# Kernel optimization log

Hardware: AMD Instinct MI355X
Metric: run time of the kernel (lower is better)

The kernel has to match this reference:

```python
import jax, jax.numpy as jnp
import numpy as np

H_DIM = 256
N_HEADS = 8
HEAD_DIM = H_DIM // N_HEADS
B, N = 2, 2048
LN_EPS = 1e-5


def setup_inputs() -> dict:
    key = jax.random.key(0)
    ks = jax.random.split(key, 20)
    s = 1.0 / np.sqrt(H_DIM)
    inp = {
        'hidden': jax.random.normal(ks[0], (B, N, H_DIM), jnp.float32),
        'adjacency': jax.random.uniform(ks[1], (B, N, N), jnp.float32),
        'positions': jax.random.uniform(ks[2], (B, N, 2), jnp.float32),
        # linear weights stored as (in, out): y = x @ W + b
        'wq': jax.random.normal(ks[3], (H_DIM, H_DIM), jnp.float32) * s,
        'bq': jnp.zeros((H_DIM,), jnp.float32),
        'wk': jax.random.normal(ks[4], (H_DIM, H_DIM), jnp.float32) * s,
        'bk': jnp.zeros((H_DIM,), jnp.float32),
        'wv': jax.random.normal(ks[5], (H_DIM, H_DIM), jnp.float32) * s,
        'bv': jnp.zeros((H_DIM,), jnp.float32),
        'wo': jax.random.normal(ks[6], (H_DIM, H_DIM), jnp.float32) * s,
        'bo': jnp.zeros((H_DIM,), jnp.float32),
        'g1': jnp.ones((H_DIM,), jnp.float32),
        'b1': jnp.zeros((H_DIM,), jnp.float32),
        'g2': jnp.ones((H_DIM,), jnp.float32),
        'b2': jnp.zeros((H_DIM,), jnp.float32),
        'w_ff1': jax.random.normal(ks[7], (H_DIM, 4 * H_DIM), jnp.float32) * s,
        'b_ff1': jnp.zeros((4 * H_DIM,), jnp.float32),
        'w_ff2': jax.random.normal(ks[8], (4 * H_DIM, H_DIM), jnp.float32) * (1.0 / np.sqrt(4 * H_DIM)),
        'b_ff2': jnp.zeros((H_DIM,), jnp.float32),
    }
    return inp


def _layernorm(x, g, b):
    mu = jnp.mean(x, axis=-1, keepdims=True)
    var = jnp.var(x, axis=-1, keepdims=True)
    return (x - mu) * jax.lax.rsqrt(var + LN_EPS) * g + b


def reference(hidden, adjacency, positions, wq, bq, wk, bk, wv, bv, wo, bo,
              g1, b1, g2, b2, w_ff1, b_ff1, w_ff2, b_ff2):
    b_, n_, _ = hidden.shape
    normalized = _layernorm(hidden, g1, b1)
    # project and split heads: [B, H, N, Dh]
    def heads(x):
        return x.reshape(b_, n_, N_HEADS, HEAD_DIM).transpose(0, 2, 1, 3)
    q = heads(normalized @ wq + bq)
    k = heads(normalized @ wk + bk)
    v = heads(normalized @ wv + bv)
    logits = jnp.einsum('bhnd,bhmd->bhnm', q, k) / np.sqrt(HEAD_DIM)
    cond = adjacency[:, None, :, :]  # mode == 'connectivity'
    logits = logits + (2.0 * cond - 1.0)
    weights = jax.nn.softmax(logits, axis=-1)
    weights = weights * (0.25 + 0.75 * cond)
    weights = weights / jnp.maximum(weights.sum(axis=-1, keepdims=True), 1e-6)
    attended = jnp.einsum('bhnm,bhmd->bhnd', weights, v)
    attended = attended.transpose(0, 2, 1, 3).reshape(b_, n_, H_DIM)
    hidden = hidden + attended @ wo + bo
    h2 = _layernorm(hidden, g2, b2)
    ff = jax.nn.gelu(h2 @ w_ff1 + b_ff1, approximate=False) @ w_ff2 + b_ff2
    return hidden + ff
```

## Files before the change

### kernel.cpp

```cpp
#include <hip/hip_runtime.h>
#include <math.h>

#define BB 2
#define NN 2048
#define HD 256
#define NH 8
#define DH 32
#define NTOK (BB*NN)
#define QKVLD 768
#define NSPLIT 2
#define KVPB (NN/NSPLIT)
#define NTILES (KVPB/64)

typedef _Float16 h8 __attribute__((ext_vector_type(8)));
typedef _Float16 h4 __attribute__((ext_vector_type(4)));
typedef float fx4 __attribute__((ext_vector_type(4)));

#define LOG2E 1.4426950408889634f
#define SQ_LOG2 0.25503486f
#define C1A (2.0f * LOG2E)
#define C0A (-(LOG2E + 6.0f))

__device__ __forceinline__ void ln_row(const float* __restrict__ x,
    const float* __restrict__ g, const float* __restrict__ bta,
    _Float16* __restrict__ yh, int row, int lane)
{
  const float* xr = x + (size_t)row * HD + lane * 4;
  float4 v = *(const float4*)xr;
  float s = v.x + v.y + v.z + v.w;
  #pragma unroll
  for (int off = 32; off > 0; off >>= 1) s += __shfl_xor(s, off);
  float mu = s * (1.0f / HD);
  float dx0 = v.x - mu, dx1 = v.y - mu, dx2 = v.z - mu, dx3 = v.w - mu;
  float ss = dx0*dx0 + dx1*dx1 + dx2*dx2 + dx3*dx3;
  #pragma unroll
  for (int off = 32; off > 0; off >>= 1) ss += __shfl_xor(ss, off);
  float rinv = rsqrtf(ss * (1.0f / HD) + 1e-5f);
  float4 gv = *(const float4*)(g   + lane * 4);
  float4 bv = *(const float4*)(bta + lane * 4);
  h4 hh;
  hh[0] = (_Float16)(dx0 * rinv * gv.x + bv.x);
  hh[1] = (_Float16)(dx1 * rinv * gv.y + bv.y);
  hh[2] = (_Float16)(dx2 * rinv * gv.z + bv.z);
  hh[3] = (_Float16)(dx3 * rinv * gv.w + bv.w);
  *(h4*)(yh + (size_t)row * HD + lane * 4) = hh;
}

__global__ __launch_bounds__(256) void ln_kernel(const float* __restrict__ x,
    const float* __restrict__ g, const float* __restrict__ bta,
    _Float16* __restrict__ yh)
{
  ln_row(x, g, bta, yh, blockIdx.x * 4 + (threadIdx.x >> 6), threadIdx.x & 63);
}

__device__ __forceinline__ void do_transpose(const float* __restrict__ W,
    _Float16* __restrict__ Wh, int Nw, int rowoff, int ldout, float scale,
    int bx, int by, float (*tile)[33])
{
  int k0 = by * 32, n0 = bx * 32;
  int c = threadIdx.x & 31, r = threadIdx.x >> 5;
  #pragma unroll
  for (int i = 0; i < 4; i++)
    tile[r + i * 8][c] = W[(size_t)(k0 + r + i * 8) * Nw + n0 + c];
  __syncthreads();
  #pragma unroll
  for (int i = 0; i < 4; i++) {
    int n = r + i * 8;
    Wh[(size_t)(rowoff + n0 + n) * ldout + k0 + c] = (_Float16)(tile[c][n] * scale);
  }
}

__global__ __launch_bounds__(256) void prep_kernel(
    const float* wq, const float* wk, const float* wv, const float* wo,
    const float* wf1, const float* wf2,
    const float* bq, const float* bk, const float* bv,
    const float* hidden, const float* g1, const float* b1,
    _Float16* WtQKVh, _Float16* WtOh, _Float16* WtF1h, _Float16* WtF2h,
    float* biasqkv, _Float16* norm1h)
{
  __shared__ float tile[32][33];
  int bid = blockIdx.x;
  if (bid < 64)        do_transpose(wq,  WtQKVh,  256,   0,  256, SQ_LOG2, bid & 7, bid >> 3, tile);
  else if (bid < 128)  do_transpose(wk,  WtQKVh,  256, 256,  256, 1.0f, (bid-64) & 7, (bid-64) >> 3, tile);
  else if (bid < 192)  do_transpose(wv,  WtQKVh,  256, 512,  256, 1.0f, (bid-128) & 7, (bid-128) >> 3, tile);
  else if (bid < 256)  do_transpose(wo,  WtOh,    256,   0,  256, 1.0f, (bid-192) & 7, (bid-192) >> 3, tile);
  else if (bid < 512)  do_transpose(wf1, WtF1h,  1024,   0,  256, 1.0f, (bid-256) & 31, (bid-256) >> 5, tile);
  else if (bid < 768)  do_transpose(wf2, WtF2h,   256,   0, 1024, 1.0f, (bid-512) & 7, (bid-512) >> 3, tile);
  else if (bid == 768) {
    #pragma unroll
    for (int j = 0; j < 3; j++) {
      int t = j * 256 + threadIdx.x;
      biasqkv[t] = (t < 256) ? bq[t] * SQ_LOG2 : (t < 512) ? bk[t - 256] : bv[t - 512];
    }
  } else {
    ln_row(hidden, g1, b1, norm1h, (bid - 769) * 4 + (threadIdx.x >> 6), threadIdx.x & 63);
  }
}

template<int KK, int NT, int NX, int ACT, int RES, int OM>
__global__ __launch_bounds__(256) void gemm16_kernel(
    const _Float16* __restrict__ Ah, const _Float16* __restrict__ Wh,
    const float* __restrict__ bias, const float* __restrict__ resid,
    float* __restrict__ Cf, _Float16* __restrict__ Ch,
    _Float16* __restrict__ vtb, int N)
{
  const int lin = blockIdx.x;
  const int qch = gridDim.x >> 3;
  const int wg = (lin & 7) * qch + (lin >> 3);
  const int bx = wg % NX, by = wg / NX;
  const int n0 = bx * (NT * 16);
  const int m0 = by * 64;
  const int t = threadIdx.x, w = t >> 6, l = t & 63;
  const int ml = l & 15, g = l >> 4;
  const int mrow = m0 + w * 16 + ml;

  const _Float16* aph = Ah + (size_t)mrow * KK + g * 8;
  const _Float16* whp[NT];
  #pragma unroll
  for (int nt = 0; nt < NT; nt++)
    whp[nt] = Wh + (size_t)(n0 + nt * 16 + ml) * KK + g * 8;

  fx4 acc[NT];
  #pragma unroll
  for (int nt = 0; nt < NT; nt++) acc[nt] = (fx4){0.f, 0.f, 0.f, 0.f};

  h8 ah = *(const h8*)(aph);
  h8 wh[NT];
  #pragma unroll
  for (int nt = 0; nt < NT; nt++) wh[nt] = *(const h8*)(whp[nt]);

  #pragma unroll 2
  for (int k0 = 32; k0 <= KK; k0 += 32) {
    h8 ahn;
    h8 whn[NT];
    if (k0 < KK) {
      ahn = *(const h8*)(aph + k0);
      #pragma unroll
      for (int nt = 0; nt < NT; nt++) whn[nt] = *(const h8*)(whp[nt] + k0);
    }
    #pragma unroll
    for (int nt = 0; nt < NT; nt++)
      acc[nt] = __builtin_amdgcn_mfma_f32_16x16x32_f16(ah, wh[nt], acc[nt], 0, 0, 0);
    ah = ahn;
    #pragma unroll
    for (int nt = 0; nt < NT; nt++) wh[nt] = whn[nt];
  }

  #pragma unroll
  for (int nt = 0; nt < NT; nt++) {
    int n = n0 + nt * 16 + ml;
    float bv = bias[n];
    #pragma unroll
    for (int i = 0; i < 4; i++) {
      int m = m0 + w * 16 + 4 * g + i;
      float vv = acc[nt][i] + bv;
      if (ACT == 1) vv = 0.5f * vv * (1.0f + erff(vv * 0.70710678118654752f));
      if (RES)      vv += resid[(size_t)m * N + n];
      if (OM == 0) {
        Cf[(size_t)m * N + n] = vv;
      } else if (OM == 1) {
        Ch[(size_t)m * N + n] = (_Float16)vv;
      } else {
        if (n < 512) Ch[(size_t)m * QKVLD + n] = (_Float16)vv;
        else {
          int dim = n - 512, kv = m & (NN - 1), bb = m >> 11;
          int kvp = (kv & ~31) | ((kv & 15) << 1) | ((kv >> 4) & 1);
          vtb[((size_t)(bb * HD + dim)) * NN + kvp] = (_Float16)vv;
        }
      }
    }
  }
}

__global__ __launch_bounds__(256) void wo_fused_kernel(
    const _Float16* __restrict__ Opart, const float* __restrict__ Spart,
    const _Float16* __restrict__ Wh, const float* __restrict__ bias,
    const float* __restrict__ resid, float* __restrict__ Cf)
{
  const int lin = blockIdx.x;
  const int qch = gridDim.x >> 3;
  const int wg = (lin & 7) * qch + (lin >> 3);
  const int bx = wg & 7, by = wg >> 3;
  const int n0 = bx * 32;
  const int m0 = by * 64;
  const int t = threadIdx.x, w = t >> 6, l = t & 63;
  const int ml = l & 15, g = l >> 4;
  const int mrow = m0 + w * 16 + ml;
  const int bb = mrow >> 11, qrow = mrow & (NN - 1);

  const _Float16* whp0 = Wh + (size_t)(n0 + ml) * HD + g * 8;
  const _Float16* whp1 = Wh + (size_t)(n0 + 16 + ml) * HD + g * 8;

  fx4 acc0 = {0.f, 0.f, 0.f, 0.f};
  fx4 acc1 = {0.f, 0.f, 0.f, 0.f};

  #pragma unroll
  for (int h = 0; h < NH; h++) {
    size_t p0 = ((size_t)((bb * 2 + 0) * NH + h)) * NN + qrow;
    size_t p1 = ((size_t)((bb * 2 + 1) * NH + h)) * NN + qrow;
    float s0 = Spart[p0], s1 = Spart[p1];
    float den = 1.0f / (s0 + s1);
    float w0 = s0 * den, w1 = s1 * den;
    h8 o0 = *(const h8*)(Opart + p0 * 32 + g * 8);
    h8 o1 = *(const h8*)(Opart + p1 * 32 + g * 8);
    h8 ah;
    #pragma unroll
    for (int j = 0; j < 8; j++)
      ah[j] = (_Float16)(w0 * (float)o0[j] + w1 * (float)o1[j]);
    h8 wh0 = *(const h8*)(whp0 + h * 32);
    h8 wh1 = *(const h8*)(whp1 + h * 32);
    acc0 = __builtin_amdgcn_mfma_f32_16x16x32_f16(ah, wh0, acc0, 0, 0, 0);
    acc1 = __builtin_amdgcn_mfma_f32_16x16x32_f16(ah, wh1, acc1, 0, 0, 0);
  }

  #pragma unroll
  for (int i = 0; i < 4; i++) {
    int m = m0 + w * 16 + 4 * g + i;
    int na = n0 + ml, nb = n0 + 16 + ml;
    Cf[(size_t)m * HD + na] = acc0[i] + bias[na] + resid[(size_t)m * HD + na];
    Cf[(size_t)m * HD + nb] = acc1[i] + bias[nb] + resid[(size_t)m * HD + nb];
  }
}

__global__ __launch_bounds__(512) void attn_mfma_kernel(
    const _Float16* __restrict__ qkv16, const _Float16* __restrict__ vtb,
    const float* __restrict__ adj,
    _Float16* __restrict__ Opart, float* __restrict__ Spart)
{
  __shared__ _Float16 Ksh[2][2][64][40];
  __shared__ _Float16 Vp[2][2][32][72];
  __shared__ _Float16 AdjL[2][64][68];

  const int z = blockIdx.z;
  const int b = z >> 1, half = z & 1;
  const int hg = blockIdx.y;
  const int q0 = blockIdx.x * 64;
  const int t = threadIdx.x;
  const int hh_ = t >> 8;
  const int head = hg * 2 + hh_;
  const int tl = t & 255;
  const int w = tl >> 6, l = t & 63;
  const int m = l & 15, g = l >> 4;
  const int kvbase = half * KVPB;

  const int qrow = q0 + w * 16 + m;
  h8 qh = *(const h8*)(qkv16 + ((size_t)(b * NN + qrow)) * QKVLD + head * DH + g * 8);

  fx4 ot0 = {0.f, 0.f, 0.f, 0.f};
  fx4 ot1 = {0.f, 0.f, 0.f, 0.f};
  float S4[4] = {0.f, 0.f, 0.f, 0.f};

  const int arow0 = t >> 4;
  const int acol = (t & 15) * 4;
  const float* adjbase = adj + ((size_t)(b * NN + q0)) * NN + kvbase;

  const int krow = tl >> 2, kd0 = (tl & 3) * 8;
  const int vdim = tl >> 3, vkc = (tl & 7) * 8;
  const _Float16* kbase = qkv16 + ((size_t)(b * NN + kvbase + krow)) * QKVLD + 256 + head * DH + kd0;
  const _Float16* vbase = vtb + ((size_t)(b * HD + head * DH + vdim)) * NN + kvbase + vkc;

  h8 kreg = *(const h8*)kbase;
  h8 vreg = *(const h8*)vbase;

  {
    float4 ar[2];
    #pragma unroll
    for (int j = 0; j < 2; j++)
      ar[j] = *(const float4*)(adjbase + (size_t)(j * 32 + arow0) * NN + acol);
    #pragma unroll
    for (int j = 0; j < 2; j++) {
      h4 hh;
      hh[0] = (_Float16)ar[j].x; hh[1] = (_Float16)ar[j].y;
      hh[2] = (_Float16)ar[j].z; hh[3] = (_Float16)ar[j].w;
      *(h4*)&AdjL[0][j * 32 + arow0][acol] = hh;
    }
  }
  *(h8*)&Ksh[hh_][0][krow][kd0] = kreg;
  *(h8*)&Vp[hh_][0][vdim][vkc]  = vreg;
  kreg = *(const h8*)(kbase + (size_t)64 * QKVLD);
  vreg = *(const h8*)(vbase + 64);
  __syncthreads();

  for (int tt = 0; tt < NTILES; ++tt) {
    const int cur = tt & 1;

    float4 ar[2];
    if (tt + 1 < NTILES) {
      #pragma unroll
      for (int j = 0; j < 2; j++)
        ar[j] = *(const float4*)(adjbase + (size_t)(j * 32 + arow0) * NN
                                 + (tt + 1) * 64 + acol);
    }

    h8 kh0 = *(const h8*)&Ksh[hh_][cur][     m][g * 8];
    h8 kh1 = *(const h8*)&Ksh[hh_][cur][16 + m][g * 8];
    h8 kh2 = *(const h8*)&Ksh[hh_][cur][32 + m][g * 8];
    h8 kh3 = *(const h8*)&Ksh[hh_][cur][48 + m][g * 8];
    fx4 z4 = {0.f, 0.f, 0.f, 0.f};
    fx4 st[4];
    st[0] = __builtin_amdgcn_mfma_f32_16x16x32_f16(kh0, qh, z4, 0, 0, 0);
    st[1] = __builtin_amdgcn_mfma_f32_16x16x32_f16(kh1, qh, z4, 0, 0, 0);
    st[2] = __builtin_amdgcn_mfma_f32_16x16x32_f16(kh2, qh, z4, 0, 0, 0);
    st[3] = __builtin_amdgcn_mfma_f32_16x16x32_f16(kh3, qh, z4, 0, 0, 0);

    float pv[16];
    #pragma unroll
    for (int p = 0; p < 4; p++) {
      h4 ah4 = *(const h4*)&AdjL[cur][w * 16 + m][p * 16 + g * 4];
      float ps = 0.f;
      #pragma unroll
      for (int i = 0; i < 4; i++) {
        float a = (float)ah4[i];
        float e = __builtin_amdgcn_exp2f(st[p][i] + C1A * a + C0A);
        float pp = (0.25f + 0.75f * a) * e;
        pv[p * 4 + i] = pp;
        ps += pp;
      }
      S4[p] += ps;
    }
    h8 ph0, ph1;
    #pragma unroll
    for (int q2 = 0; q2 < 4; q2++) {
      ph0[2*q2]     = (_Float16)pv[q2];
      ph0[2*q2 + 1] = (_Float16)pv[4 + q2];
      ph1[2*q2]     = (_Float16)pv[8 + q2];
      ph1[2*q2 + 1] = (_Float16)pv[12 + q2];
    }

    h8 v00 = *(const h8*)&Vp[hh_][cur][m][g * 8];
    h8 v01 = *(const h8*)&Vp[hh_][cur][m][32 + g * 8];
    h8 v10 = *(const h8*)&Vp[hh_][cur][16 + m][g * 8];
    h8 v11 = *(const h8*)&Vp[hh_][cur][16 + m][32 + g * 8];
    ot0 = __builtin_amdgcn_mfma_f32_16x16x32_f16(v00, ph0, ot0, 0, 0, 0);
    ot0 = __builtin_amdgcn_mfma_f32_16x16x32_f16(v01, ph1, ot0, 0, 0, 0);
    ot1 = __builtin_amdgcn_mfma_f32_16x16x32_f16(v10, ph0, ot1, 0, 0, 0);
    ot1 = __builtin_amdgcn_mfma_f32_16x16x32_f16(v11, ph1, ot1, 0, 0, 0);

    if (tt + 1 < NTILES) {
      #pragma unroll
      for (int j = 0; j < 2; j++) {
        h4 hh;
        hh[0] = (_Float16)ar[j].x; hh[1] = (_Float16)ar[j].y;
        hh[2] = (_Float16)ar[j].z; hh[3] = (_Float16)ar[j].w;
        *(h4*)&AdjL[cur ^ 1][j * 32 + arow0][acol] = hh;
      }
      *(h8*)&Ksh[hh_][cur ^ 1][krow][kd0] = kreg;
      *(h8*)&Vp[hh_][cur ^ 1][vdim][vkc]  = vreg;
      if (tt + 2 < NTILES) {
        kreg = *(const h8*)(kbase + (size_t)((tt + 2) * 64) * QKVLD);
        vreg = *(const h8*)(vbase + (tt + 2) * 64);
      }
    }
    __syncthreads();
  }

  float S = (S4[0] + S4[1]) + (S4[2] + S4[3]);
  S += __shfl_xor(S, 16);
  S += __shfl_xor(S, 32);

  float is = 1.0f / S;
  size_t prow = ((size_t)(z * NH + head)) * NN + qrow;
  _Float16* po = Opart + prow * 32;
  h4 o0h, o1h;
  #pragma unroll
  for (int j = 0; j < 4; j++) {
    o0h[j] = (_Float16)(ot0[j] * is);
    o1h[j] = (_Float16)(ot1[j] * is);
  }
  *(h4*)(po + 4 * g)      = o0h;
  *(h4*)(po + 16 + 4 * g) = o1h;
  if (g == 0) Spart[prow] = S;
}

extern "C" void kernel_launch(void* const* d_in, const int* in_sizes, int n_in,
                              void* d_out, int out_size, void* d_ws, size_t ws_size,
                              hipStream_t stream)
{
  const float* hidden    = (const float*)d_in[0];
  const float* adjacency = (const float*)d_in[1];
  const float* wq  = (const float*)d_in[3];
  const float* bq  = (const float*)d_in[4];
  const float* wk  = (const float*)d_in[5];
  const float* bk  = (const float*)d_in[6];
  const float* wv  = (const float*)d_in[7];
  const float* bv  = (const float*)d_in[8];
  const float* wo  = (const float*)d_in[9];
  const float* bo  = (const float*)d_in[10];
  const float* g1  = (const float*)d_in[11];
  const float* b1  = (const float*)d_in[12];
  const float* g2  = (const float*)d_in[13];
  const float* b2  = (const float*)d_in[14];
  const float* wf1 = (const float*)d_in[15];
  const float* bf1 = (const float*)d_in[16];
  const float* wf2 = (const float*)d_in[17];
  const float* bf2 = (const float*)d_in[18];
  float* out = (float*)d_out;

  char* base = (char*)d_ws;
  const size_t MB = 1024 * 1024;
  _Float16* norm1h = (_Float16*)(base);
  _Float16* qkv16  = (_Float16*)(base + 2*MB);
  _Float16* vtb    = (_Float16*)(base + 8*MB);
  float*    hid2   = (float*)(base + 12*MB);
  _Float16* Opart = (_Float16*)(base + 16*MB);
  _Float16* ffah  = (_Float16*)(base + 16*MB);
  float* Spart = (float*)(base + 25*MB);
  _Float16* wtb = (_Float16*)(base + 26*MB);
  _Float16* WtQKVh = wtb; wtb += 768 * 256;
  _Float16* WtOh   = wtb; wtb += 256 * 256;
  _Float16* WtF1h  = wtb; wtb += 1024 * 256;
  _Float16* WtF2h  = wtb; wtb += 256 * 1024;
  float* biasqkv = (float*)(base + 28*MB);

  prep_kernel<<<1793, 256, 0, stream>>>(wq, wk, wv, wo, wf1, wf2, bq, bk, bv,
      hidden, g1, b1, WtQKVh, WtOh, WtF1h, WtF2h, biasqkv, norm1h);

  gemm16_kernel<256, 4, 12, 0, 0, 2><<<768, 256, 0, stream>>>(
      norm1h, WtQKVh, biasqkv, nullptr, nullptr, qkv16, vtb, QKVLD);

  attn_mfma_kernel<<<dim3(NN / 64, NH / 2, BB * NSPLIT), 512, 0, stream>>>(
      qkv16, vtb, adjacency, Opart, Spart);

  wo_fused_kernel<<<512, 256, 0, stream>>>(
      Opart, Spart, WtOh, bo, hidden, hid2);

  ln_kernel<<<NTOK / 4, 256, 0, stream>>>(hid2, g2, b2, norm1h);

  gemm16_kernel<256, 4, 16, 1, 0, 1><<<1024, 256, 0, stream>>>(
      norm1h, WtF1h, bf1, nullptr, nullptr, ffah, nullptr, 1024);

  gemm16_kernel<1024, 4, 4, 0, 1, 0><<<256, 256, 0, stream>>>(
      ffah, WtF2h, bf2, hid2, out, nullptr, nullptr, 256);
}
```

Measured before the change: 112.7 us.

## Drop KV split in attention and use generic GEMM for output projection

Removes the two-way split of the key/value range in attention, so each block processes the full sequence and writes final normalized head outputs directly into a token-major fp16 buffer. The custom wo_fused kernel that merged partial outputs with their softmax sums is replaced by the generic gemm16 kernel, with bias and residual added. This drops the partial-output writes and reads and the merge arithmetic. In exchange the attention grid is halved to 256 blocks, each with twice the serial KV loop, which may reduce occupancy and latency hiding on a device with many CUs.

```diff
diff --git a/kernel.cpp b/kernel.cpp
--- a/kernel.cpp
+++ b/kernel.cpp
@@ -8,9 +8,7 @@
 #define DH 32
 #define NTOK (BB*NN)
 #define QKVLD 768
-#define NSPLIT 2
-#define KVPB (NN/NSPLIT)
-#define NTILES (KVPB/64)
+#define NTILES (NN/64)
 
 typedef _Float16 h8 __attribute__((ext_vector_type(8)));
 typedef _Float16 h4 __attribute__((ext_vector_type(4)));
@@ -172,67 +170,15 @@
   }
 }
 
-__global__ __launch_bounds__(256) void wo_fused_kernel(
-    const _Float16* __restrict__ Opart, const float* __restrict__ Spart,
-    const _Float16* __restrict__ Wh, const float* __restrict__ bias,
-    const float* __restrict__ resid, float* __restrict__ Cf)
-{
-  const int lin = blockIdx.x;
-  const int qch = gridDim.x >> 3;
-  const int wg = (lin & 7) * qch + (lin >> 3);
-  const int bx = wg & 7, by = wg >> 3;
-  const int n0 = bx * 32;
-  const int m0 = by * 64;
-  const int t = threadIdx.x, w = t >> 6, l = t & 63;
-  const int ml = l & 15, g = l >> 4;
-  const int mrow = m0 + w * 16 + ml;
-  const int bb = mrow >> 11, qrow = mrow & (NN - 1);
-
-  const _Float16* whp0 = Wh + (size_t)(n0 + ml) * HD + g * 8;
-  const _Float16* whp1 = Wh + (size_t)(n0 + 16 + ml) * HD + g * 8;
-
-  fx4 acc0 = {0.f, 0.f, 0.f, 0.f};
-  fx4 acc1 = {0.f, 0.f, 0.f, 0.f};
-
-  #pragma unroll
-  for (int h = 0; h < NH; h++) {
-    size_t p0 = ((size_t)((bb * 2 + 0) * NH + h)) * NN + qrow;
-    size_t p1 = ((size_t)((bb * 2 + 1) * NH + h)) * NN + qrow;
-    float s0 = Spart[p0], s1 = Spart[p1];
-    float den = 1.0f / (s0 + s1);
-    float w0 = s0 * den, w1 = s1 * den;
-    h8 o0 = *(const h8*)(Opart + p0 * 32 + g * 8);
-    h8 o1 = *(const h8*)(Opart + p1 * 32 + g * 8);
-    h8 ah;
-    #pragma unroll
-    for (int j = 0; j < 8; j++)
-      ah[j] = (_Float16)(w0 * (float)o0[j] + w1 * (float)o1[j]);
-    h8 wh0 = *(const h8*)(whp0 + h * 32);
-    h8 wh1 = *(const h8*)(whp1 + h * 32);
-    acc0 = __builtin_amdgcn_mfma_f32_16x16x32_f16(ah, wh0, acc0, 0, 0, 0);
-    acc1 = __builtin_amdgcn_mfma_f32_16x16x32_f16(ah, wh1, acc1, 0, 0, 0);
-  }
-
-  #pragma unroll
-  for (int i = 0; i < 4; i++) {
-    int m = m0 + w * 16 + 4 * g + i;
-    int na = n0 + ml, nb = n0 + 16 + ml;
-    Cf[(size_t)m * HD + na] = acc0[i] + bias[na] + resid[(size_t)m * HD + na];
-    Cf[(size_t)m * HD + nb] = acc1[i] + bias[nb] + resid[(size_t)m * HD + nb];
-  }
-}
-
 __global__ __launch_bounds__(512) void attn_mfma_kernel(
     const _Float16* __restrict__ qkv16, const _Float16* __restrict__ vtb,
-    const float* __restrict__ adj,
-    _Float16* __restrict__ Opart, float* __restrict__ Spart)
+    const float* __restrict__ adj, _Float16* __restrict__ atth)
 {
   __shared__ _Float16 Ksh[2][2][64][40];
   __shared__ _Float16 Vp[2][2][32][72];
   __shared__ _Float16 AdjL[2][64][68];
 
-  const int z = blockIdx.z;
-  const int b = z >> 1, half = z & 1;
+  const int b = blockIdx.z;
   const int hg = blockIdx.y;
   const int q0 = blockIdx.x * 64;
   const int t = threadIdx.x;
@@ -241,7 +187,6 @@
   const int tl = t & 255;
   const int w = tl >> 6, l = t & 63;
   const int m = l & 15, g = l >> 4;
-  const int kvbase = half * KVPB;
 
   const int qrow = q0 + w * 16 + m;
   h8 qh = *(const h8*)(qkv16 + ((size_t)(b * NN + qrow)) * QKVLD + head * DH + g * 8);
@@ -252,12 +197,12 @@
 
   const int arow0 = t >> 4;
   const int acol = (t & 15) * 4;
-  const float* adjbase = adj + ((size_t)(b * NN + q0)) * NN + kvbase;
+  const float* adjbase = adj + ((size_t)(b * NN + q0)) * NN;
 
   const int krow = tl >> 2, kd0 = (tl & 3) * 8;
   const int vdim = tl >> 3, vkc = (tl & 7) * 8;
-  const _Float16* kbase = qkv16 + ((size_t)(b * NN + kvbase + krow)) * QKVLD + 256 + head * DH + kd0;
-  const _Float16* vbase = vtb + ((size_t)(b * HD + head * DH + vdim)) * NN + kvbase + vkc;
+  const _Float16* kbase = qkv16 + ((size_t)(b * NN + krow)) * QKVLD + 256 + head * DH + kd0;
+  const _Float16* vbase = vtb + ((size_t)(b * HD + head * DH + vdim)) * NN + vkc;
 
   h8 kreg = *(const h8*)kbase;
   h8 vreg = *(const h8*)vbase;
@@ -359,17 +304,15 @@
   S += __shfl_xor(S, 32);
 
   float is = 1.0f / S;
-  size_t prow = ((size_t)(z * NH + head)) * NN + qrow;
-  _Float16* po = Opart + prow * 32;
+  _Float16* ao = atth + ((size_t)(b * NN + qrow)) * HD + head * DH;
   h4 o0h, o1h;
   #pragma unroll
   for (int j = 0; j < 4; j++) {
     o0h[j] = (_Float16)(ot0[j] * is);
     o1h[j] = (_Float16)(ot1[j] * is);
   }
-  *(h4*)(po + 4 * g)      = o0h;
-  *(h4*)(po + 16 + 4 * g) = o1h;
-  if (g == 0) Spart[prow] = S;
+  *(h4*)(ao + 4 * g)      = o0h;
+  *(h4*)(ao + 16 + 4 * g) = o1h;
 }
 
 extern "C" void kernel_launch(void* const* d_in, const int* in_sizes, int n_in,
@@ -401,10 +344,9 @@
   _Float16* norm1h = (_Float16*)(base);
   _Float16* qkv16  = (_Float16*)(base + 2*MB);
   _Float16* vtb    = (_Float16*)(base + 8*MB);
+  _Float16* atth   = (_Float16*)(base + 10*MB);
   float*    hid2   = (float*)(base + 12*MB);
-  _Float16* Opart = (_Float16*)(base + 16*MB);
-  _Float16* ffah  = (_Float16*)(base + 16*MB);
-  float* Spart = (float*)(base + 25*MB);
+  _Float16* ffah   = (_Float16*)(base + 16*MB);
   _Float16* wtb = (_Float16*)(base + 26*MB);
   _Float16* WtQKVh = wtb; wtb += 768 * 256;
   _Float16* WtOh   = wtb; wtb += 256 * 256;
@@ -418,11 +360,11 @@
   gemm16_kernel<256, 4, 12, 0, 0, 2><<<768, 256, 0, stream>>>(
       norm1h, WtQKVh, biasqkv, nullptr, nullptr, qkv16, vtb, QKVLD);
 
-  attn_mfma_kernel<<<dim3(NN / 64, NH / 2, BB * NSPLIT), 512, 0, stream>>>(
-      qkv16, vtb, adjacency, Opart, Spart);
-
-  wo_fused_kernel<<<512, 256, 0, stream>>>(
-      Opart, Spart, WtOh, bo, hidden, hid2);
+  attn_mfma_kernel<<<dim3(NN / 64, NH / 2, BB), 512, 0, stream>>>(
+      qkv16, vtb, adjacency, atth);
+
+  gemm16_kernel<256, 2, 8, 0, 1, 0><<<512, 256, 0, stream>>>(
+      atth, WtOh, bo, hidden, hid2, nullptr, nullptr, 256);
 
   ln_kernel<<<NTOK / 4, 256, 0, stream>>>(hid2, g2, b2, norm1h);
 
```

New measurement: 113.1 us. Within noise of the previous version (+0.4%).
